# Optimization experiments

Hardware: AMD Instinct MI355X
Metric: run time of the kernel (lower is better)

## Reference

```python
import jax, jax.numpy as jnp
import numpy as np

N_NODES = 50000
N_EDGES = 800000
DIM = 64
BN_EPS = 1e-5


def setup_inputs() -> dict:
    key = jax.random.key(0)
    ks = jax.random.split(key, 9)
    s = 1.0 / np.sqrt(DIM)
    feature = jax.random.normal(ks[0], (N_NODES, DIM), jnp.float32)
    edge_index = jax.random.randint(ks[1], (2, N_EDGES), 0, N_NODES)
    Wk = jax.random.normal(ks[2], (DIM, DIM), jnp.float32) * s
    Wq = jax.random.normal(ks[3], (DIM, DIM), jnp.float32) * s
    Wv = jax.random.normal(ks[4], (DIM, DIM), jnp.float32) * s
    bk = jax.random.normal(ks[5], (DIM,), jnp.float32) * 0.01
    bq = jax.random.normal(ks[6], (DIM,), jnp.float32) * 0.01
    bv = jax.random.normal(ks[7], (DIM,), jnp.float32) * 0.01
    bias = jax.random.normal(ks[8], (DIM,), jnp.float32) * 0.01
    gamma = jnp.ones((DIM,), jnp.float32)
    beta = jnp.zeros((DIM,), jnp.float32)
    return dict(feature=feature, edge_index=edge_index, Wk=Wk, bk=bk,
                Wq=Wq, bq=bq, Wv=Wv, bv=bv, bias=bias, gamma=gamma, beta=beta)


def reference(feature, edge_index, Wk, bk, Wq, bq, Wv, bv, bias, gamma, beta):
    # Node-level projections (dense GEMMs on [N, D])
    K = feature @ Wk + bk   # applied to x_i (dst)
    Q = feature @ Wq + bq   # applied to x_j (src)
    V = feature @ Wv + bv   # applied to x_j (src)
    src, dst = edge_index[0], edge_index[1]
    # Per-edge gather -> sigmoid gate -> gated message  [E, D]
    eta = jax.nn.sigmoid(K[dst] + Q[src])
    msg = eta * V[src]
    # Scatter-add into destination nodes  [N, D]
    agg = jax.ops.segment_sum(msg, dst, num_segments=feature.shape[0])
    h = agg + bias
    # BatchNorm1d over nodes (batch statistics, biased variance) + ReLU
    mean = jnp.mean(h, axis=0)
    var = jnp.var(h, axis=0)
    h = (h - mean) * jax.lax.rsqrt(var + BN_EPS) * gamma + beta
    return jax.nn.relu(h)
```

## Files before the change

### kernel.cpp

```cpp
#include <hip/hip_runtime.h>
#include <hip/hip_fp16.h>
#include <stdint.h>

#define N_NODES 50000
#define N_EDGES 800000
#define DIM 64
#define BN_EPS 1e-5f
#define CAP 64
#define ZERO_NODE N_NODES
#define POISON 0xAAAAAAAAu

#define PROJ_BLOCKS 2346
#define FUSED_BLOCKS 2737
#define NTILES 3125
#define AGG_BLOCKS 1024

__global__ __launch_bounds__(256) void proj_scatter_kernel(
    const float* __restrict__ feat,
    const float* __restrict__ Wk, const float* __restrict__ bk,
    const float* __restrict__ Wq, const float* __restrict__ bq,
    const float* __restrict__ Wv, const float* __restrict__ bv,
    float* __restrict__ K, __half* __restrict__ QV,
    const int* __restrict__ ei, uint32_t* __restrict__ counts,
    uint16_t* __restrict__ bucket)
{
  __shared__ float sW[DIM][DIM];
  __shared__ float sf[64][DIM + 4];
  __shared__ float sb[DIM];

  const int b = blockIdx.x;
  const int tid = threadIdx.x;

  if (b % 7 == 6) {
    const int base = (b / 7) * 2048 + tid * 8;
    if (base >= N_EDGES) return;
    if (base + 8 <= N_EDGES) {
      const int4 s0 = *(const int4*)(ei + base);
      const int4 s1 = *(const int4*)(ei + base + 4);
      const int4 d0 = *(const int4*)(ei + N_EDGES + base);
      const int4 d1 = *(const int4*)(ei + N_EDGES + base + 4);
      const int ss[8] = {s0.x, s0.y, s0.z, s0.w, s1.x, s1.y, s1.z, s1.w};
      const int dd[8] = {d0.x, d0.y, d0.z, d0.w, d1.x, d1.y, d1.z, d1.w};
      uint32_t pos[8];
#pragma unroll
      for (int i = 0; i < 8; ++i)
        pos[i] = atomicAdd(&counts[dd[i]], 1u) - POISON;
#pragma unroll
      for (int i = 0; i < 8; ++i)
        if (pos[i] < CAP) bucket[(size_t)dd[i] * CAP + pos[i]] = (uint16_t)ss[i];
    } else {
      for (int e = base; e < N_EDGES; ++e) {
        const int src = ei[e];
        const int dst = ei[N_EDGES + e];
        const uint32_t pos = atomicAdd(&counts[dst], 1u) - POISON;
        if (pos < CAP) bucket[(size_t)dst * CAP + pos] = (uint16_t)src;
      }
    }
    return;
  }

  const int pidx = b - b / 7;
  const int mat = pidx % 3;
  const int tile = pidx / 3;
  const float* __restrict__ W = (mat == 0) ? Wk : (mat == 1) ? Wq : Wv;
  const float* __restrict__ bb = (mat == 0) ? bk : (mat == 1) ? bq : bv;

  {
    const float4* w4 = (const float4*)W;
    float4* s4 = (float4*)&sW[0][0];
    for (int i = tid; i < DIM * DIM / 4; i += 256) s4[i] = w4[i];
  }
  if (tid < DIM) sb[tid] = bb[tid];

  const int node0 = tile * 64;
  for (int i = tid; i < 64 * 16; i += 256) {
    const int n = i >> 4, d4 = i & 15;
    const int gn = node0 + n;
    float4 v = make_float4(0.f, 0.f, 0.f, 0.f);
    if (gn < N_NODES) v = ((const float4*)feat)[gn * 16 + d4];
    *(float4*)&sf[n][d4 * 4] = v;
  }
  __syncthreads();

  const int t = tid & 15;
  const int g = tid >> 4;

  float4 a[4];
  const float4 bias = *(const float4*)&sb[t * 4];
#pragma unroll
  for (int m = 0; m < 4; ++m) a[m] = bias;

  const float4* sW4 = (const float4*)&sW[0][0];
  for (int d4 = 0; d4 < 16; ++d4) {
    const float4 w0 = sW4[(4 * d4 + 0) * 16 + t];
    const float4 w1 = sW4[(4 * d4 + 1) * 16 + t];
    const float4 w2 = sW4[(4 * d4 + 2) * 16 + t];
    const float4 w3 = sW4[(4 * d4 + 3) * 16 + t];
#pragma unroll
    for (int m = 0; m < 4; ++m) {
      const float4 f = *(const float4*)&sf[g + 16 * m][4 * d4];
      a[m].x += f.x * w0.x + f.y * w1.x + f.z * w2.x + f.w * w3.x;
      a[m].y += f.x * w0.y + f.y * w1.y + f.z * w2.y + f.w * w3.y;
      a[m].z += f.x * w0.z + f.y * w1.z + f.z * w2.z + f.w * w3.z;
      a[m].w += f.x * w0.w + f.y * w1.w + f.z * w2.w + f.w * w3.w;
    }
  }

  if (mat == 0) {
#pragma unroll
    for (int m = 0; m < 4; ++m) {
      const int gn = node0 + g + 16 * m;
      if (gn < N_NODES) ((float4*)K)[gn * 16 + t] = a[m];
    }
  } else {
    const int part = (mat == 1) ? 0 : 16;
#pragma unroll
    for (int m = 0; m < 4; ++m) {
      const int gn = node0 + g + 16 * m;
      if (gn <= N_NODES) {
        union { __half2 h[2]; uint2 u; } pk;
        pk.h[0] = __floats2half2_rn(a[m].x, a[m].y);
        pk.h[1] = __floats2half2_rn(a[m].z, a[m].w);
        if (gn == N_NODES) { pk.u.x = 0u; pk.u.y = 0u; }
        ((uint2*)QV)[gn * 32 + part + t] = pk.u;
      }
    }
  }
}

__device__ __forceinline__ float4 edge_acc(float4 acc, const float4 k,
                                           const uint2 qu, const uint2 vu)
{
  union { uint2 u; __half2 h[2]; } q, v;
  q.u = qu; v.u = vu;
  const float2 q0 = __half22float2(q.h[0]);
  const float2 q1 = __half22float2(q.h[1]);
  const float2 v0 = __half22float2(v.h[0]);
  const float2 v1 = __half22float2(v.h[1]);
  acc.x += v0.x * __builtin_amdgcn_rcpf(1.0f + __expf(-(k.x + q0.x)));
  acc.y += v0.y * __builtin_amdgcn_rcpf(1.0f + __expf(-(k.y + q0.y)));
  acc.z += v1.x * __builtin_amdgcn_rcpf(1.0f + __expf(-(k.z + q1.x)));
  acc.w += v1.y * __builtin_amdgcn_rcpf(1.0f + __expf(-(k.w + q1.y)));
  return acc;
}

__global__ __launch_bounds__(256) void aggregate_kernel(
    const uint32_t* __restrict__ counts, const uint16_t* __restrict__ bucket,
    const float4* __restrict__ K4, const uint2* __restrict__ QV2,
    float4* __restrict__ agg4, float* __restrict__ stats)
{
  const int tid = threadIdx.x;
  const int row = tid >> 4;
  const int t = tid & 15;

  float4 psum = make_float4(0.f, 0.f, 0.f, 0.f);
  float4 pssq = make_float4(0.f, 0.f, 0.f, 0.f);

  for (int tile = blockIdx.x; tile < NTILES; tile += AGG_BLOCKS) {
    const int n = tile * 16 + row;
    const float4 k = K4[n * 16 + t];
    int deg = (int)(counts[n] - POISON);
    if (deg > CAP) deg = CAP;
    const uint16_t* bp = bucket + (size_t)n * CAP;
    float4 acc = make_float4(0.f, 0.f, 0.f, 0.f);

    for (int j0 = 0; j0 < deg; j0 += 16) {
      const int navail = deg - j0;
      const int s = (t < navail) ? (int)bp[j0 + t] : ZERO_NODE;

      int sA[8]; uint2 qA[8], vA[8];
#pragma unroll
      for (int i = 0; i < 8; ++i) sA[i] = __shfl(s, i, 16);
#pragma unroll
      for (int i = 0; i < 8; ++i) {
        qA[i] = QV2[sA[i] * 32 + t];
        vA[i] = QV2[sA[i] * 32 + 16 + t];
      }

      const bool haveB = navail > 8;
      int sB[8]; uint2 qB[8], vB[8];
      if (haveB) {
#pragma unroll
        for (int i = 0; i < 8; ++i) sB[i] = __shfl(s, 8 + i, 16);
#pragma unroll
        for (int i = 0; i < 8; ++i) {
          qB[i] = QV2[sB[i] * 32 + t];
          vB[i] = QV2[sB[i] * 32 + 16 + t];
        }
      }

#pragma unroll
      for (int i = 0; i < 8; ++i) acc = edge_acc(acc, k, qA[i], vA[i]);
      if (haveB) {
#pragma unroll
        for (int i = 0; i < 8; ++i) acc = edge_acc(acc, k, qB[i], vB[i]);
      }
    }
    agg4[n * 16 + t] = acc;
    psum.x += acc.x; psum.y += acc.y; psum.z += acc.z; psum.w += acc.w;
    pssq.x += acc.x * acc.x; pssq.y += acc.y * acc.y;
    pssq.z += acc.z * acc.z; pssq.w += acc.w * acc.w;
  }

  __shared__ float sred[2][16][DIM + 4];
  *(float4*)&sred[0][row][t * 4] = psum;
  *(float4*)&sred[1][row][t * 4] = pssq;
  __syncthreads();
  if (tid < 128) {
    const int s = tid >> 6, c = tid & 63;
    float v = 0.0f;
#pragma unroll
    for (int r = 0; r < 16; ++r) v += sred[s][r][c];
    atomicAdd(&stats[tid], v);
  }
}

__global__ __launch_bounds__(256) void out_kernel(
    float* __restrict__ out, const float* __restrict__ stats,
    const float* __restrict__ gamma, const float* __restrict__ beta)
{
  const int idx = blockIdx.x * 256 + threadIdx.x;
  if (idx >= N_NODES * (DIM / 4)) return;
  const int t = idx & 15;
  const float4 v = ((const float4*)out)[idx];
  const float invN = 1.0f / (float)N_NODES;
  const float vin[4] = { v.x, v.y, v.z, v.w };
  float o[4];
#pragma unroll
  for (int j = 0; j < 4; ++j) {
    const int c = t * 4 + j;
    const float mean = stats[c] * invN;
    float var = stats[DIM + c] * invN - mean * mean;
    var = var < 0.0f ? 0.0f : var;
    const float scale = rsqrtf(var + BN_EPS) * gamma[c];
    const float shift = beta[c] - mean * scale;
    const float x = vin[j] * scale + shift;
    o[j] = x > 0.0f ? x : 0.0f;
  }
  float4 r; r.x = o[0]; r.y = o[1]; r.z = o[2]; r.w = o[3];
  ((float4*)out)[idx] = r;
}

extern "C" void kernel_launch(void* const* d_in, const int* in_sizes, int n_in,
                              void* d_out, int out_size, void* d_ws, size_t ws_size,
                              hipStream_t stream) {
  (void)in_sizes; (void)n_in; (void)out_size; (void)ws_size;
  const float* feat  = (const float*)d_in[0];
  const int*   ei    = (const int*)d_in[1];
  const float* Wk    = (const float*)d_in[2];
  const float* bk    = (const float*)d_in[3];
  const float* Wq    = (const float*)d_in[4];
  const float* bq    = (const float*)d_in[5];
  const float* Wv    = (const float*)d_in[6];
  const float* bv    = (const float*)d_in[7];
  const float* gamma = (const float*)d_in[9];
  const float* beta  = (const float*)d_in[10];

  char* base = (char*)d_ws;
  float*    K      = (float*)base;
  __half*   QV     = (__half*)(base + 12800000);
  float*    stats  = (float*)(base + 25600256);
  uint32_t* counts = (uint32_t*)(base + 25600768);
  uint16_t* bucket = (uint16_t*)(base + 25800768);

  proj_scatter_kernel<<<FUSED_BLOCKS, 256, 0, stream>>>(
      feat, Wk, bk, Wq, bq, Wv, bv, K, QV, ei, counts, bucket);

  aggregate_kernel<<<AGG_BLOCKS, 256, 0, stream>>>(
      counts, bucket, (const float4*)K, (const uint2*)QV, (float4*)d_out,
      stats);

  out_kernel<<<(N_NODES * (DIM / 4) + 255) / 256, 256, 0, stream>>>(
      (float*)d_out, stats, gamma, beta);
}
```

Before: 175.1 us.

## Fuse aggregation and batchnorm into persistent kernel with grid barrier

```diff
diff --git a/kernel.cpp b/kernel.cpp
--- a/kernel.cpp
+++ b/kernel.cpp
@@ -14,6 +14,7 @@
 #define FUSED_BLOCKS 2737
 #define NTILES 3125
 #define AGG_BLOCKS 1024
+#define MAX_TILES 8
 
 __global__ __launch_bounds__(256) void proj_scatter_kernel(
     const float* __restrict__ feat,
@@ -144,6 +145,134 @@
   return acc;
 }
 
+__device__ __forceinline__ float4 agg_tile(
+    int n, int t, const uint32_t* __restrict__ counts,
+    const uint16_t* __restrict__ bucket, const float4* __restrict__ K4,
+    const uint2* __restrict__ QV2)
+{
+  const float4 k = K4[n * 16 + t];
+  int deg = (int)(counts[n] - POISON);
+  if (deg > CAP) deg = CAP;
+  const uint16_t* bp = bucket + (size_t)n * CAP;
+  float4 acc = make_float4(0.f, 0.f, 0.f, 0.f);
+
+  for (int j0 = 0; j0 < deg; j0 += 16) {
+    const int navail = deg - j0;
+    const int s = (t < navail) ? (int)bp[j0 + t] : ZERO_NODE;
+
+    int sA[8]; uint2 qA[8], vA[8];
+#pragma unroll
+    for (int i = 0; i < 8; ++i) sA[i] = __shfl(s, i, 16);
+#pragma unroll
+    for (int i = 0; i < 8; ++i) {
+      qA[i] = QV2[sA[i] * 32 + t];
+      vA[i] = QV2[sA[i] * 32 + 16 + t];
+    }
+    const bool haveB = navail > 8;
+    int sB[8]; uint2 qB[8], vB[8];
+    if (haveB) {
+#pragma unroll
+      for (int i = 0; i < 8; ++i) sB[i] = __shfl(s, 8 + i, 16);
+#pragma unroll
+      for (int i = 0; i < 8; ++i) {
+        qB[i] = QV2[sB[i] * 32 + t];
+        vB[i] = QV2[sB[i] * 32 + 16 + t];
+      }
+    }
+#pragma unroll
+    for (int i = 0; i < 8; ++i) acc = edge_acc(acc, k, qA[i], vA[i]);
+    if (haveB) {
+#pragma unroll
+      for (int i = 0; i < 8; ++i) acc = edge_acc(acc, k, qB[i], vB[i]);
+    }
+  }
+  return acc;
+}
+
+__global__ __launch_bounds__(256, 4) void agg_bn_kernel(
+    const uint32_t* __restrict__ counts, const uint16_t* __restrict__ bucket,
+    const float4* __restrict__ K4, const uint2* __restrict__ QV2,
+    const float* __restrict__ gamma, const float* __restrict__ beta,
+    float* __restrict__ stats, uint32_t* __restrict__ bar,
+    float4* __restrict__ out4, int nblk)
+{
+  const int tid = threadIdx.x;
+  const int row = tid >> 4;
+  const int t = tid & 15;
+
+  float4 acc[MAX_TILES];
+  float4 psum = make_float4(0.f, 0.f, 0.f, 0.f);
+  float4 pssq = make_float4(0.f, 0.f, 0.f, 0.f);
+
+#pragma unroll
+  for (int i = 0; i < MAX_TILES; ++i) {
+    const int tile = blockIdx.x + i * nblk;
+    acc[i] = make_float4(0.f, 0.f, 0.f, 0.f);
+    if (tile < NTILES) {
+      acc[i] = agg_tile(tile * 16 + row, t, counts, bucket, K4, QV2);
+      psum.x += acc[i].x; psum.y += acc[i].y;
+      psum.z += acc[i].z; psum.w += acc[i].w;
+      pssq.x += acc[i].x * acc[i].x; pssq.y += acc[i].y * acc[i].y;
+      pssq.z += acc[i].z * acc[i].z; pssq.w += acc[i].w * acc[i].w;
+    }
+  }
+
+  __shared__ float sred[2][16][DIM + 4];
+  *(float4*)&sred[0][row][t * 4] = psum;
+  *(float4*)&sred[1][row][t * 4] = pssq;
+  __syncthreads();
+  if (tid < 128) {
+    const int s = tid >> 6, c = tid & 63;
+    float v = 0.0f;
+#pragma unroll
+    for (int r = 0; r < 16; ++r) v += sred[s][r][c];
+    atomicAdd(&stats[tid], v);
+  }
+
+  __syncthreads();
+  if (tid == 0) {
+    __threadfence();
+    __hip_atomic_fetch_add(bar, 1u, __ATOMIC_ACQ_REL, __HIP_MEMORY_SCOPE_AGENT);
+    const uint32_t target = POISON + (uint32_t)nblk;
+    while (__hip_atomic_load(bar, __ATOMIC_ACQUIRE, __HIP_MEMORY_SCOPE_AGENT)
+           < target)
+      __builtin_amdgcn_s_sleep(2);
+  }
+  __syncthreads();
+
+  __shared__ float sstat[128];
+  if (tid < 128)
+    sstat[tid] = __hip_atomic_load(&stats[tid], __ATOMIC_RELAXED,
+                                   __HIP_MEMORY_SCOPE_AGENT);
+  __syncthreads();
+
+  const float invN = 1.0f / (float)N_NODES;
+  float scale[4], shift[4];
+#pragma unroll
+  for (int j = 0; j < 4; ++j) {
+    const int c = t * 4 + j;
+    const float mean = sstat[c] * invN;
+    float var = sstat[DIM + c] * invN - mean * mean;
+    var = var < 0.0f ? 0.0f : var;
+    scale[j] = rsqrtf(var + BN_EPS) * gamma[c];
+    shift[j] = beta[c] - mean * scale[j];
+  }
+
+#pragma unroll
+  for (int i = 0; i < MAX_TILES; ++i) {
+    const int tile = blockIdx.x + i * nblk;
+    if (tile < NTILES) {
+      const int n = tile * 16 + row;
+      float4 r;
+      r.x = acc[i].x * scale[0] + shift[0]; r.x = r.x > 0.f ? r.x : 0.f;
+      r.y = acc[i].y * scale[1] + shift[1]; r.y = r.y > 0.f ? r.y : 0.f;
+      r.z = acc[i].z * scale[2] + shift[2]; r.z = r.z > 0.f ? r.z : 0.f;
+      r.w = acc[i].w * scale[3] + shift[3]; r.w = r.w > 0.f ? r.w : 0.f;
+      out4[n * 16 + t] = r;
+    }
+  }
+}
+
 __global__ __launch_bounds__(256) void aggregate_kernel(
     const uint32_t* __restrict__ counts, const uint16_t* __restrict__ bucket,
     const float4* __restrict__ K4, const uint2* __restrict__ QV2,
@@ -157,46 +286,8 @@
   float4 pssq = make_float4(0.f, 0.f, 0.f, 0.f);
 
   for (int tile = blockIdx.x; tile < NTILES; tile += AGG_BLOCKS) {
-    const int n = tile * 16 + row;
-    const float4 k = K4[n * 16 + t];
-    int deg = (int)(counts[n] - POISON);
-    if (deg > CAP) deg = CAP;
-    const uint16_t* bp = bucket + (size_t)n * CAP;
-    float4 acc = make_float4(0.f, 0.f, 0.f, 0.f);
-
-    for (int j0 = 0; j0 < deg; j0 += 16) {
-      const int navail = deg - j0;
-      const int s = (t < navail) ? (int)bp[j0 + t] : ZERO_NODE;
-
-      int sA[8]; uint2 qA[8], vA[8];
-#pragma unroll
-      for (int i = 0; i < 8; ++i) sA[i] = __shfl(s, i, 16);
-#pragma unroll
-      for (int i = 0; i < 8; ++i) {
-        qA[i] = QV2[sA[i] * 32 + t];
-        vA[i] = QV2[sA[i] * 32 + 16 + t];
-      }
-
-      const bool haveB = navail > 8;
-      int sB[8]; uint2 qB[8], vB[8];
-      if (haveB) {
-#pragma unroll
-        for (int i = 0; i < 8; ++i) sB[i] = __shfl(s, 8 + i, 16);
-#pragma unroll
-        for (int i = 0; i < 8; ++i) {
-          qB[i] = QV2[sB[i] * 32 + t];
-          vB[i] = QV2[sB[i] * 32 + 16 + t];
-        }
-      }
-
-#pragma unroll
-      for (int i = 0; i < 8; ++i) acc = edge_acc(acc, k, qA[i], vA[i]);
-      if (haveB) {
-#pragma unroll
-        for (int i = 0; i < 8; ++i) acc = edge_acc(acc, k, qB[i], vB[i]);
-      }
-    }
-    agg4[n * 16 + t] = acc;
+    const float4 acc = agg_tile(tile * 16 + row, t, counts, bucket, K4, QV2);
+    agg4[(tile * 16 + row) * 16 + t] = acc;
     psum.x += acc.x; psum.y += acc.y; psum.z += acc.z; psum.w += acc.w;
     pssq.x += acc.x * acc.x; pssq.y += acc.y * acc.y;
     pssq.z += acc.z * acc.z; pssq.w += acc.w * acc.w;
@@ -260,16 +351,29 @@
   float*    K      = (float*)base;
   __half*   QV     = (__half*)(base + 12800000);
   float*    stats  = (float*)(base + 25600256);
-  uint32_t* counts = (uint32_t*)(base + 25600768);
-  uint16_t* bucket = (uint16_t*)(base + 25800768);
+  uint32_t* bar    = (uint32_t*)(base + 25600768);
+  uint32_t* counts = (uint32_t*)(base + 25600832);
+  uint16_t* bucket = (uint16_t*)(base + 25800832);
 
   proj_scatter_kernel<<<FUSED_BLOCKS, 256, 0, stream>>>(
       feat, Wk, bk, Wq, bq, Wv, bv, K, QV, ei, counts, bucket);
 
-  aggregate_kernel<<<AGG_BLOCKS, 256, 0, stream>>>(
-      counts, bucket, (const float4*)K, (const uint2*)QV, (float4*)d_out,
-      stats);
-
-  out_kernel<<<(N_NODES * (DIM / 4) + 255) / 256, 256, 0, stream>>>(
-      (float*)d_out, stats, gamma, beta);
-}
+  int mb = 0;
+  if (hipOccupancyMaxActiveBlocksPerMultiprocessor(&mb, agg_bn_kernel, 256, 0)
+          != hipSuccess)
+    mb = 0;
+
+  if (mb >= 2) {
+    int nblk = mb * 256;
+    if (nblk > 1024) nblk = 1024;
+    agg_bn_kernel<<<nblk, 256, 0, stream>>>(
+        counts, bucket, (const float4*)K, (const uint2*)QV,
+        gamma, beta, stats, bar, (float4*)d_out, nblk);
+  } else {
+    aggregate_kernel<<<AGG_BLOCKS, 256, 0, stream>>>(
+        counts, bucket, (const float4*)K, (const uint2*)QV, (float4*)d_out,
+        stats);
+    out_kernel<<<(N_NODES * (DIM / 4) + 255) / 256, 256, 0, stream>>>(
+        (float*)d_out, stats, gamma, beta);
+  }
+}
```

New measurement: 249.5 us. +42.5%, slower.
